# Kernel optimization log

Hardware: AMD Instinct MI355X
Metric: run time of the kernel (lower is better)

Reference implementation:

```python
import jax, jax.numpy as jnp
import numpy as np

N_HEAD = 16
RMS_EPS = 1.1920928955078125e-07  # torch float32 finfo eps (F.rms_norm default)


def _apply_rotary(x, cos, sin):
    # x: [B,T,H,D], cos/sin: [1,T,1,D/2]
    d = x.shape[-1] // 2
    x1, x2 = x[..., :d], x[..., d:]
    return jnp.concatenate([x1 * cos + x2 * sin, -x1 * sin + x2 * cos], axis=-1)


def _rms_norm(x):
    var = jnp.mean(jnp.square(x), axis=-1, keepdims=True)
    return x * jax.lax.rsqrt(var + RMS_EPS)


def setup_inputs() -> dict:
    key = jax.random.key(0)
    ks = jax.random.split(key, 5)
    B, T, C, H = 2, 2048, 1024, N_HEAD
    D = C // H
    x = jax.random.normal(ks[0], (B, T, C), dtype=jnp.float32)
    cos = jax.random.uniform(ks[1], (1, T, 1, D // 2), dtype=jnp.float32)
    sin = jax.random.uniform(ks[2], (1, T, 1, D // 2), dtype=jnp.float32)
    kv_w = jax.random.normal(ks[3], (C, C), dtype=jnp.float32) * (C ** -0.5)
    proj_w = jax.random.normal(ks[4], (C, C), dtype=jnp.float32) * (C ** -0.5)
    return {"x": x, "cos": cos, "sin": sin, "kv_w": kv_w, "proj_w": proj_w, "window_left": 1024}


def reference(x, cos, sin, kv_w, proj_w, window_left):
    B, T, C = x.shape
    H = N_HEAD
    D = C // H
    scale = D ** -0.5

    q = x.reshape(B, T, H, D)                       # no Q projection
    kv = (x @ kv_w.T).reshape(B, T, H, D)           # tied K=V projection

    q = _rms_norm(_apply_rotary(q, cos, sin))
    kv = _rms_norm(_apply_rotary(kv, cos, sin))

    # scores: [B,H,T,T]
    scores = jnp.einsum('bqhd,bkhd->bhqk', q, kv) * scale

    pos = jnp.arange(T)
    dist = pos[:, None] - pos[None, :]              # query_pos - key_pos
    allowed = (dist >= 0) & (dist <= window_left)   # causal + sliding window
    scores = jnp.where(allowed[None, None], scores, -jnp.inf)

    attn = jax.nn.softmax(scores, axis=-1)
    out = jnp.einsum('bhqk,bkhd->bqhd', attn, kv).reshape(B, T, C)
    return out @ proj_w.T
```

## Files before the change

kernel.cpp:

```cpp
#include <hip/hip_runtime.h>
#include <hip/hip_bf16.h>

using u16 = unsigned short;
typedef __attribute__((ext_vector_type(8))) short short8v;
typedef __attribute__((ext_vector_type(4))) float f32x4;

#define MFMA16(a, b, c) __builtin_amdgcn_mfma_f32_16x16x32_bf16((a), (b), (c), 0, 0, 0)

#define GLOAD16(g, l) __builtin_amdgcn_global_load_lds(                       \
    (const __attribute__((address_space(1))) void*)(const void*)(g),          \
    (__attribute__((address_space(3))) void*)(void*)(l), 16, 0, 0)

static __device__ __forceinline__ u16 f2bf(float x) {
  __hip_bfloat16 h = __float2bfloat16(x);
  return __builtin_bit_cast(u16, h);
}

__global__ __launch_bounds__(256) void cast2_f32_bf16(const float* __restrict__ a, u16* __restrict__ da,
                                                      const float* __restrict__ b, u16* __restrict__ db) {
  int bid = blockIdx.x;
  const float* s; u16* d; int i;
  if (bid < 1024) { s = a; d = da; i = bid; }
  else            { s = b; d = db; i = bid - 1024; }
  int idx = (i * 256 + threadIdx.x) * 4;
  float4 v = *reinterpret_cast<const float4*>(s + idx);
  ushort4 o;
  o.x = f2bf(v.x); o.y = f2bf(v.y); o.z = f2bf(v.z); o.w = f2bf(v.w);
  *reinterpret_cast<ushort4*>(d + idx) = o;
}

__global__ __launch_bounds__(256) void reduce2(const float* __restrict__ p0,
                                               const float* __restrict__ p1,
                                               float* __restrict__ out) {
  int i = (blockIdx.x * 256 + threadIdx.x) * 4;
  float4 a = *reinterpret_cast<const float4*>(p0 + i);
  float4 b = *reinterpret_cast<const float4*>(p1 + i);
  float4 o = {a.x + b.x, a.y + b.y, a.z + b.z, a.w + b.w};
  *reinterpret_cast<float4*>(out + i) = o;
}

__global__ __launch_bounds__(256) void gemm_bt(const u16* __restrict__ A,
                                               const u16* __restrict__ Bt,
                                               float* __restrict__ C,
                                               int M, int N, int K, int K2) {
  __shared__ u16 As[4][64 * 32];
  __shared__ u16 Bs[4][128 * 32];
  unsigned flat = blockIdx.y * gridDim.x + blockIdx.x;
  unsigned nwg = gridDim.x * gridDim.y;
  unsigned swz = (flat & 7) * (nwg >> 3) + (flat >> 3);
  int bm = swz % gridDim.x, bn = swz / gridDim.x;
  int z = blockIdx.z;
  int tid = threadIdx.x;
  int wid = tid >> 6, l = tid & 63, lr = l & 15, lg = l >> 4;
  int wr = wid >> 1, wc = wid & 1;

  int srow = l >> 2, scol = (l & 3) * 8;
  const u16* Ag  = A  + (size_t)(bm * 64 + wid * 16 + srow) * K + z * K2 + scol;
  const u16* Bg0 = Bt + (size_t)(bn * 128 + wid * 32 + srow) * K + z * K2 + scol;
  const u16* Bg1 = Bg0 + (size_t)16 * K;
  C += (size_t)z * M * N;

  f32x4 acc[2][4];
#pragma unroll
  for (int m = 0; m < 2; m++)
#pragma unroll
    for (int n = 0; n < 4; n++) acc[m][n] = (f32x4){0.f, 0.f, 0.f, 0.f};

  const int NT = K2 >> 5;

#pragma unroll
  for (int t = 0; t < 2; t++) {
    GLOAD16(Ag + t * 32, &As[t][wid * 512]);
    GLOAD16(Bg0 + t * 32, &Bs[t][wid * 1024]);
    GLOAD16(Bg1 + t * 32, &Bs[t][wid * 1024 + 512]);
  }

  for (int t = 0; t < NT; t++) {
    int cur = t & 3;
    if (t + 2 < NT) {
      int nb = (t + 2) & 3;
      int ko = (t + 2) * 32;
      GLOAD16(Ag + ko, &As[nb][wid * 512]);
      GLOAD16(Bg0 + ko, &Bs[nb][wid * 1024]);
      GLOAD16(Bg1 + ko, &Bs[nb][wid * 1024 + 512]);
    }
    if (t + 2 < NT)      asm volatile("s_waitcnt vmcnt(6)" ::: "memory");
    else if (t + 1 < NT) asm volatile("s_waitcnt vmcnt(3)" ::: "memory");
    else                 asm volatile("s_waitcnt vmcnt(0)" ::: "memory");
    __builtin_amdgcn_s_barrier();

    short8v af[2], bfr[4];
#pragma unroll
    for (int m = 0; m < 2; m++)
      af[m] = *reinterpret_cast<const short8v*>(&As[cur][(wr * 32 + m * 16 + lr) * 32 + lg * 8]);
#pragma unroll
    for (int n = 0; n < 4; n++)
      bfr[n] = *reinterpret_cast<const short8v*>(&Bs[cur][(wc * 64 + n * 16 + lr) * 32 + lg * 8]);
    asm volatile("s_waitcnt lgkmcnt(0)" ::: "memory");
    __builtin_amdgcn_sched_barrier(0);
    __builtin_amdgcn_s_setprio(1);
#pragma unroll
    for (int m = 0; m < 2; m++)
#pragma unroll
      for (int n = 0; n < 4; n++) acc[m][n] = MFMA16(af[m], bfr[n], acc[m][n]);
    __builtin_amdgcn_s_setprio(0);
  }

#pragma unroll
  for (int m = 0; m < 2; m++)
#pragma unroll
    for (int n = 0; n < 4; n++)
#pragma unroll
      for (int r = 0; r < 4; r++) {
        int row = bm * 64 + wr * 32 + m * 16 + lg * 4 + r;
        int col = bn * 128 + wc * 64 + n * 16 + lr;
        C[(size_t)row * N + col] = acc[m][n][r];
      }
}

__global__ __launch_bounds__(256) void rope_rms_x(const float* __restrict__ src,
                                                  u16* __restrict__ xbf,
                                                  u16* __restrict__ qdst,
                                                  const float* __restrict__ cosp,
                                                  const float* __restrict__ sinp,
                                                  float scale) {
  int R = blockIdx.x * 4 + (threadIdx.x >> 6);
  int l = threadIdx.x & 63;
  int h = R & 15;
  int bt = R >> 4;
  int t = bt & 2047, b = bt >> 11;

  float v = src[((size_t)R << 6) + l];
  xbf[((size_t)R << 6) + l] = f2bf(v);
  float p = __shfl_xor(v, 32);
  float c = cosp[(t << 5) + (l & 31)];
  float s = sinp[(t << 5) + (l & 31)];
  float r = v * c + ((l < 32) ? p * s : -p * s);
  float sq = r * r;
  sq += __shfl_xor(sq, 32);
  sq += __shfl_xor(sq, 16);
  sq += __shfl_xor(sq, 8);
  sq += __shfl_xor(sq, 4);
  sq += __shfl_xor(sq, 2);
  sq += __shfl_xor(sq, 1);
  float inv = rsqrtf(sq * (1.0f / 64.0f) + 1.1920928955078125e-07f) * scale;
  qdst[((((size_t)b * 16 + h) * 2048 + t) << 6) + l] = f2bf(r * inv);
}

__global__ __launch_bounds__(256) void rope_rms_kv(const float* __restrict__ srcP0,
                                                   const float* __restrict__ srcP1,
                                                   u16* __restrict__ dst,
                                                   u16* __restrict__ dstT,
                                                   const float* __restrict__ cosp,
                                                   const float* __restrict__ sinp) {
  __shared__ u16 Ld[64][72];
  int t0 = blockIdx.x << 6;
  int bh = blockIdx.y;
  int b = bh >> 4, h = bh & 15;
  int tid = threadIdx.x;
  int w = tid >> 6, l = tid & 63;

  for (int i = 0; i < 16; i++) {
    int tt = w * 16 + i;
    int t = t0 + tt;
    size_t idx = ((((size_t)b * 2048 + t) * 16 + h) << 6) + l;
    float v = srcP0[idx] + srcP1[idx];
    float p = __shfl_xor(v, 32);
    float cl = cosp[(t << 5) + (l & 31)];
    float sl = sinp[(t << 5) + (l & 31)];
    float r = v * cl + ((l < 32) ? p * sl : -p * sl);
    float sq = r * r;
    sq += __shfl_xor(sq, 32);
    sq += __shfl_xor(sq, 16);
    sq += __shfl_xor(sq, 8);
    sq += __shfl_xor(sq, 4);
    sq += __shfl_xor(sq, 2);
    sq += __shfl_xor(sq, 1);
    float inv = rsqrtf(sq * (1.0f / 64.0f) + 1.1920928955078125e-07f);
    u16 val = f2bf(r * inv);
    dst[(((size_t)bh * 2048 + t) << 6) + l] = val;
    Ld[tt][l] = val;
  }
  __syncthreads();
#pragma unroll
  for (int i = 0; i < 2; i++) {
    int c = tid + i * 256, dr = c >> 3, sg = c & 7;
    short8v v;
#pragma unroll
    for (int j = 0; j < 8; j++) v[j] = (short)Ld[sg * 8 + j][dr];
    *reinterpret_cast<short8v*>(dstT + ((size_t)bh * 64 + dr) * 2048 + t0 + sg * 8) = v;
  }
}

__global__ __launch_bounds__(256) void attn_swa(const u16* __restrict__ Q,
                                                const u16* __restrict__ KV,
                                                const u16* __restrict__ KVt,
                                                u16* __restrict__ O,
                                                const int* __restrict__ winp) {
  const int T = 2048;
  int bid = blockIdx.x;
  int bh = bid & 31;
  int qi = 31 - (bid >> 5);
  int q0 = qi << 6;
  int b = bh >> 4, h = bh & 15;
  int W = *winp;
  int tid = threadIdx.x;
  int wid = tid >> 6, l = tid & 63, lr = l & 15, lg = l >> 4;

  __shared__ u16 Kl[64][72];
  __shared__ u16 Vt[64][72];
  __shared__ u16 Pl[4][16][72];

  const u16* Qb = Q + (((size_t)bh * T + q0 + wid * 16 + lr) << 6);
  short8v aq0 = *reinterpret_cast<const short8v*>(Qb + lg * 8);
  short8v aq1 = *reinterpret_cast<const short8v*>(Qb + 32 + lg * 8);

  const short one_bf = (short)0x3F80;
  short8v vones = {one_bf, one_bf, one_bf, one_bf, one_bf, one_bf, one_bf, one_bf};

  float l_run[4];
  f32x4 oacc[4];
#pragma unroll
  for (int r = 0; r < 4; r++) l_run[r] = 0.f;
#pragma unroll
  for (int dt = 0; dt < 4; dt++) oacc[dt] = (f32x4){0.f, 0.f, 0.f, 0.f};

  int lo = q0 - W;
  if (lo < 0) lo = 0;
  lo &= ~63;

  const u16* KVbh  = KV + (((size_t)bh * T) << 6);
  const u16* KVtbh = KVt + ((size_t)bh << 6) * T;
  int r8 = tid >> 3, sg = tid & 7;

  short8v vK0 = *reinterpret_cast<const short8v*>(KVbh + ((size_t)(lo + r8) << 6) + sg * 8);
  short8v vK1 = *reinterpret_cast<const short8v*>(KVbh + ((size_t)(lo + r8 + 32) << 6) + sg * 8);
  short8v vV0 = *reinterpret_cast<const short8v*>(KVtbh + (size_t)r8 * T + lo + sg * 8);
  short8v vV1 = *reinterpret_cast<const short8v*>(KVtbh + (size_t)(r8 + 32) * T + lo + sg * 8);

  for (int kt = lo; kt <= q0; kt += 64) {
    __syncthreads();
    *reinterpret_cast<short8v*>(&Kl[r8][sg * 8]) = vK0;
    *reinterpret_cast<short8v*>(&Kl[r8 + 32][sg * 8]) = vK1;
    *reinterpret_cast<short8v*>(&Vt[r8][sg * 8]) = vV0;
    *reinterpret_cast<short8v*>(&Vt[r8 + 32][sg * 8]) = vV1;
    __syncthreads();
    if (kt < q0) {
      vK0 = *reinterpret_cast<const short8v*>(KVbh + ((size_t)(kt + 64 + r8) << 6) + sg * 8);
      vK1 = *reinterpret_cast<const short8v*>(KVbh + ((size_t)(kt + 64 + r8 + 32) << 6) + sg * 8);
      vV0 = *reinterpret_cast<const short8v*>(KVtbh + (size_t)r8 * T + kt + 64 + sg * 8);
      vV1 = *reinterpret_cast<const short8v*>(KVtbh + (size_t)(r8 + 32) * T + kt + 64 + sg * 8);
    }

    f32x4 s[4];
#pragma unroll
    for (int nt = 0; nt < 4; nt++) {
      s[nt] = (f32x4){0.f, 0.f, 0.f, 0.f};
      short8v b0 = *reinterpret_cast<const short8v*>(&Kl[nt * 16 + lr][lg * 8]);
      s[nt] = MFMA16(aq0, b0, s[nt]);
      short8v b1 = *reinterpret_cast<const short8v*>(&Kl[nt * 16 + lr][32 + lg * 8]);
      s[nt] = MFMA16(aq1, b1, s[nt]);
    }

    bool edge = (kt + 63 > q0 + wid * 16) || ((q0 - kt) + wid * 16 + 15 > W);
#pragma unroll
    for (int r = 0; r < 4; r++) {
      if (edge) {
        int t = q0 + wid * 16 + lg * 4 + r;
#pragma unroll
        for (int nt = 0; nt < 4; nt++) {
          int k = kt + nt * 16 + lr;
          float val = ((k <= t) && (t - k <= W)) ? s[nt][r] : -1e30f;
          Pl[wid][lg * 4 + r][nt * 16 + lr] = f2bf(exp2f(val - 12.f));
        }
      } else {
#pragma unroll
        for (int nt = 0; nt < 4; nt++)
          Pl[wid][lg * 4 + r][nt * 16 + lr] = f2bf(exp2f(s[nt][r] - 12.f));
      }
    }

    short8v ap0 = *reinterpret_cast<const short8v*>(&Pl[wid][lr][lg * 8]);
    short8v ap1 = *reinterpret_cast<const short8v*>(&Pl[wid][lr][32 + lg * 8]);
    f32x4 psum = (f32x4){0.f, 0.f, 0.f, 0.f};
    psum = MFMA16(ap0, vones, psum);
    psum = MFMA16(ap1, vones, psum);
#pragma unroll
    for (int dt = 0; dt < 4; dt++) {
      short8v v0 = *reinterpret_cast<const short8v*>(&Vt[dt * 16 + lr][lg * 8]);
      oacc[dt] = MFMA16(ap0, v0, oacc[dt]);
      short8v v1 = *reinterpret_cast<const short8v*>(&Vt[dt * 16 + lr][32 + lg * 8]);
      oacc[dt] = MFMA16(ap1, v1, oacc[dt]);
    }
#pragma unroll
    for (int r = 0; r < 4; r++) l_run[r] += psum[r];
  }

#pragma unroll
  for (int r = 0; r < 4; r++) {
    int t = q0 + wid * 16 + lg * 4 + r;
    float inv = 1.f / l_run[r];
#pragma unroll
    for (int dt = 0; dt < 4; dt++) {
      O[(((size_t)b * T + t) << 10) + (h << 6) + dt * 16 + lr] = f2bf(oacc[dt][r] * inv);
    }
  }
}

extern "C" void kernel_launch(void* const* d_in, const int* in_sizes, int n_in,
                              void* d_out, int out_size, void* d_ws, size_t ws_size,
                              hipStream_t stream) {
  (void)in_sizes; (void)n_in; (void)out_size; (void)ws_size;
  const float* x    = (const float*)d_in[0];
  const float* cosp = (const float*)d_in[1];
  const float* sinp = (const float*)d_in[2];
  const float* kvw  = (const float*)d_in[3];
  const float* pw   = (const float*)d_in[4];
  const int*   win  = (const int*)d_in[5];

  char* w = (char*)d_ws;
  u16*   xbf   = (u16*)(w);
  u16*   kvwbf = (u16*)(w + (8u << 20));
  u16*   pwbf  = (u16*)(w + (10u << 20));
  float* kvfp  = (float*)(w + (12u << 20));
  float* outp  = (float*)(w + (12u << 20));
  u16*   kvbf  = (u16*)(w + (44u << 20));
  u16*   kvt   = (u16*)(w + (52u << 20));
  u16*   qbf   = (u16*)(w + (60u << 20));
  u16*   aout  = (u16*)(w + (68u << 20));
  const size_t PART = (size_t)4096 * 1024;

  cast2_f32_bf16<<<2048, 256, 0, stream>>>(kvw, kvwbf, pw, pwbf);

  rope_rms_x<<<16384, 256, 0, stream>>>(x, xbf, qbf, cosp, sinp, 0.18033688011112042f);

  gemm_bt<<<dim3(64, 8, 2), 256, 0, stream>>>(xbf, kvwbf, kvfp, 4096, 1024, 1024, 512);

  rope_rms_kv<<<dim3(32, 32), 256, 0, stream>>>(kvfp, kvfp + PART, kvbf, kvt, cosp, sinp);

  attn_swa<<<1024, 256, 0, stream>>>(qbf, kvbf, kvt, aout, win);

  gemm_bt<<<dim3(64, 8, 2), 256, 0, stream>>>(aout, pwbf, outp, 4096, 1024, 1024, 512);
  reduce2<<<4096, 256, 0, stream>>>(outp, outp + PART, (float*)d_out);
}
```

Baseline: 192.5 us.

## Drop split-K in both GEMMs and write KV projection in bf16

Both projection GEMMs move from a 2-way split-K grid (1024 blocks, fp32 partials) to a single full-K pass over 512 blocks with a new XCD-aware tile swizzle. This removes the reduce2 kernel and the fp32 partial-sum traffic. The KV GEMM now stores bf16 directly, so rope_rms_kv reads half the bytes and no longer sums partials, and the output GEMM writes straight to the output buffer. The cost is fewer blocks with twice the K loop each, which lowers occupancy on a large-CU device. Rounding the KV projection to bf16 before RoPE/RMS also adds a small precision loss.

```diff
diff --git a/kernel.cpp b/kernel.cpp
--- a/kernel.cpp
+++ b/kernel.cpp
@@ -14,6 +14,10 @@
 static __device__ __forceinline__ u16 f2bf(float x) {
   __hip_bfloat16 h = __float2bfloat16(x);
   return __builtin_bit_cast(u16, h);
+}
+static __device__ __forceinline__ float bf2f(u16 v) {
+  __hip_bfloat16 h = __builtin_bit_cast(__hip_bfloat16, v);
+  return __bfloat162float(h);
 }
 
 __global__ __launch_bounds__(256) void cast2_f32_bf16(const float* __restrict__ a, u16* __restrict__ da,
@@ -29,36 +33,24 @@
   *reinterpret_cast<ushort4*>(d + idx) = o;
 }
 
-__global__ __launch_bounds__(256) void reduce2(const float* __restrict__ p0,
-                                               const float* __restrict__ p1,
-                                               float* __restrict__ out) {
-  int i = (blockIdx.x * 256 + threadIdx.x) * 4;
-  float4 a = *reinterpret_cast<const float4*>(p0 + i);
-  float4 b = *reinterpret_cast<const float4*>(p1 + i);
-  float4 o = {a.x + b.x, a.y + b.y, a.z + b.z, a.w + b.w};
-  *reinterpret_cast<float4*>(out + i) = o;
-}
-
+template <bool BF16OUT>
 __global__ __launch_bounds__(256) void gemm_bt(const u16* __restrict__ A,
                                                const u16* __restrict__ Bt,
-                                               float* __restrict__ C,
-                                               int M, int N, int K, int K2) {
+                                               void* __restrict__ Cv,
+                                               int M, int N, int K) {
   __shared__ u16 As[4][64 * 32];
   __shared__ u16 Bs[4][128 * 32];
-  unsigned flat = blockIdx.y * gridDim.x + blockIdx.x;
-  unsigned nwg = gridDim.x * gridDim.y;
-  unsigned swz = (flat & 7) * (nwg >> 3) + (flat >> 3);
-  int bm = swz % gridDim.x, bn = swz / gridDim.x;
-  int z = blockIdx.z;
+  int bid = blockIdx.x;
+  int bm = (bid & 7) * 8 + (bid >> 6);
+  int bn = (bid >> 3) & 7;
   int tid = threadIdx.x;
   int wid = tid >> 6, l = tid & 63, lr = l & 15, lg = l >> 4;
   int wr = wid >> 1, wc = wid & 1;
 
   int srow = l >> 2, scol = (l & 3) * 8;
-  const u16* Ag  = A  + (size_t)(bm * 64 + wid * 16 + srow) * K + z * K2 + scol;
-  const u16* Bg0 = Bt + (size_t)(bn * 128 + wid * 32 + srow) * K + z * K2 + scol;
+  const u16* Ag  = A  + (size_t)(bm * 64 + wid * 16 + srow) * K + scol;
+  const u16* Bg0 = Bt + (size_t)(bn * 128 + wid * 32 + srow) * K + scol;
   const u16* Bg1 = Bg0 + (size_t)16 * K;
-  C += (size_t)z * M * N;
 
   f32x4 acc[2][4];
 #pragma unroll
@@ -66,7 +58,7 @@
 #pragma unroll
     for (int n = 0; n < 4; n++) acc[m][n] = (f32x4){0.f, 0.f, 0.f, 0.f};
 
-  const int NT = K2 >> 5;
+  const int NT = K >> 5;
 
 #pragma unroll
   for (int t = 0; t < 2; t++) {
@@ -114,7 +106,10 @@
       for (int r = 0; r < 4; r++) {
         int row = bm * 64 + wr * 32 + m * 16 + lg * 4 + r;
         int col = bn * 128 + wc * 64 + n * 16 + lr;
-        C[(size_t)row * N + col] = acc[m][n][r];
+        if constexpr (BF16OUT)
+          ((u16*)Cv)[(size_t)row * N + col] = f2bf(acc[m][n][r]);
+        else
+          ((float*)Cv)[(size_t)row * N + col] = acc[m][n][r];
       }
 }
 
@@ -147,8 +142,7 @@
   qdst[((((size_t)b * 16 + h) * 2048 + t) << 6) + l] = f2bf(r * inv);
 }
 
-__global__ __launch_bounds__(256) void rope_rms_kv(const float* __restrict__ srcP0,
-                                                   const float* __restrict__ srcP1,
+__global__ __launch_bounds__(256) void rope_rms_kv(const u16* __restrict__ src,
                                                    u16* __restrict__ dst,
                                                    u16* __restrict__ dstT,
                                                    const float* __restrict__ cosp,
@@ -164,7 +158,7 @@
     int tt = w * 16 + i;
     int t = t0 + tt;
     size_t idx = ((((size_t)b * 2048 + t) * 16 + h) << 6) + l;
-    float v = srcP0[idx] + srcP1[idx];
+    float v = bf2f(src[idx]);
     float p = __shfl_xor(v, 32);
     float cl = cosp[(t << 5) + (l & 31)];
     float sl = sinp[(t << 5) + (l & 31)];
@@ -319,27 +313,24 @@
   const int*   win  = (const int*)d_in[5];
 
   char* w = (char*)d_ws;
-  u16*   xbf   = (u16*)(w);
-  u16*   kvwbf = (u16*)(w + (8u << 20));
-  u16*   pwbf  = (u16*)(w + (10u << 20));
-  float* kvfp  = (float*)(w + (12u << 20));
-  float* outp  = (float*)(w + (12u << 20));
-  u16*   kvbf  = (u16*)(w + (44u << 20));
-  u16*   kvt   = (u16*)(w + (52u << 20));
-  u16*   qbf   = (u16*)(w + (60u << 20));
-  u16*   aout  = (u16*)(w + (68u << 20));
-  const size_t PART = (size_t)4096 * 1024;
+  u16* xbf   = (u16*)(w);
+  u16* kvwbf = (u16*)(w + (8u << 20));
+  u16* pwbf  = (u16*)(w + (10u << 20));
+  u16* kvlin = (u16*)(w + (12u << 20));
+  u16* kvbf  = (u16*)(w + (20u << 20));
+  u16* kvt   = (u16*)(w + (28u << 20));
+  u16* qbf   = (u16*)(w + (36u << 20));
+  u16* aout  = (u16*)(w + (44u << 20));
 
   cast2_f32_bf16<<<2048, 256, 0, stream>>>(kvw, kvwbf, pw, pwbf);
 
   rope_rms_x<<<16384, 256, 0, stream>>>(x, xbf, qbf, cosp, sinp, 0.18033688011112042f);
 
-  gemm_bt<<<dim3(64, 8, 2), 256, 0, stream>>>(xbf, kvwbf, kvfp, 4096, 1024, 1024, 512);
-
-  rope_rms_kv<<<dim3(32, 32), 256, 0, stream>>>(kvfp, kvfp + PART, kvbf, kvt, cosp, sinp);
+  gemm_bt<true><<<512, 256, 0, stream>>>(xbf, kvwbf, kvlin, 4096, 1024, 1024);
+
+  rope_rms_kv<<<dim3(32, 32), 256, 0, stream>>>(kvlin, kvbf, kvt, cosp, sinp);
 
   attn_swa<<<1024, 256, 0, stream>>>(qbf, kvbf, kvt, aout, win);
 
-  gemm_bt<<<dim3(64, 8, 2), 256, 0, stream>>>(aout, pwbf, outp, 4096, 1024, 1024, 512);
-  reduce2<<<4096, 256, 0, stream>>>(outp, outp + PART, (float*)d_out);
-}
+  gemm_bt<false><<<512, 256, 0, stream>>>(aout, pwbf, d_out, 4096, 1024, 1024);
+}
```

After: 168.2 us. 12.6% less time.
